# Performance work log

Measured on AMD Instinct MI355X. Metric: run time of the kernel, lower is better.

## Reference

```python
import jax, jax.numpy as jnp
import numpy as np

N = 50000       # nodes
E = 800000      # edges (before self-loops)
IN_DIM = 128
HID = 64
HEADS = 4
C = HID // HEADS  # 16 per-head channels
NEG_SLOPE = 0.2   # PyG GATConv default
BN_EPS = 1e-5


def setup_inputs() -> dict:
    key = jax.random.key(0)
    ks = jax.random.split(key, 16)
    inp = {
        "x": jax.random.normal(ks[0], (N, IN_DIM), jnp.float32),
        "edge_index": jax.random.randint(ks[1], (2, E), 0, N, dtype=jnp.int32),
    }
    def glorot(k, shape):
        fan = sum(shape)
        return jax.random.normal(k, shape, jnp.float32) * jnp.sqrt(2.0 / fan)
    # layer 0: in=IN_DIM, layer 1: in=HID
    inp["W0"] = glorot(ks[2], (IN_DIM, HEADS * C))
    inp["a_src0"] = glorot(ks[3], (HEADS, C))
    inp["a_dst0"] = glorot(ks[4], (HEADS, C))
    inp["b0"] = jnp.zeros((HEADS * C,), jnp.float32)
    inp["g0"] = jnp.ones((HID,), jnp.float32)
    inp["be0"] = jnp.zeros((HID,), jnp.float32)
    inp["W1"] = glorot(ks[5], (HID, HEADS * C))
    inp["a_src1"] = glorot(ks[6], (HEADS, C))
    inp["a_dst1"] = glorot(ks[7], (HEADS, C))
    inp["b1"] = jnp.zeros((HEADS * C,), jnp.float32)
    inp["g1"] = jnp.ones((HID,), jnp.float32)
    inp["be1"] = jnp.zeros((HID,), jnp.float32)
    return inp


def _segment_softmax(e, dst, n):
    # softmax over edges grouped by destination node, per head. e: [Et, H]
    m = jax.ops.segment_max(e, dst, num_segments=n)          # [N, H]
    ex = jnp.exp(e - m[dst])
    s = jax.ops.segment_sum(ex, dst, num_segments=n)         # [N, H]
    return ex / (s[dst] + 1e-16)


def _gat_conv(h, src, dst, W, a_s, a_d, b):
    n = h.shape[0]
    hp = (h @ W).reshape(n, HEADS, C)                        # [N, H, C]
    al_s = jnp.einsum('nhc,hc->nh', hp, a_s)                 # [N, H]
    al_d = jnp.einsum('nhc,hc->nh', hp, a_d)
    e = jax.nn.leaky_relu(al_s[src] + al_d[dst], NEG_SLOPE)  # [Et, H]
    alpha = _segment_softmax(e, dst, n)
    msg = hp[src] * alpha[:, :, None]                        # [Et, H, C]
    out = jax.ops.segment_sum(msg, dst, num_segments=n)      # [N, H, C]
    return out.reshape(n, HEADS * C) + b


def _batch_norm(h, g, b):
    mu = h.mean(axis=0)
    var = h.var(axis=0)
    return (h - mu) * jax.lax.rsqrt(var + BN_EPS) * g + b


def reference(x, edge_index, W0, a_src0, a_dst0, b0, g0, be0,
              W1, a_src1, a_dst1, b1, g1, be1):
    n = x.shape[0]
    loops = jnp.arange(n, dtype=edge_index.dtype)
    src = jnp.concatenate([edge_index[0], loops])  # PyG adds self-loops
    dst = jnp.concatenate([edge_index[1], loops])
    h = _gat_conv(x, src, dst, W0, a_src0, a_dst0, b0)
    h = _batch_norm(h, g0, be0)
    h = jax.nn.relu(h)  # dropout: identity (eval / deterministic)
    h = _gat_conv(h, src, dst, W1, a_src1, a_dst1, b1)
    h = _batch_norm(h, g1, be1)
    return h
```

## Files before the change

### kernel.cpp

```cpp
#include <hip/hip_runtime.h>

#define CAP 128

template<int K, bool APPLY_BN>
__global__ void __launch_bounds__(256, 4)
gemm_tiled(const float* __restrict__ X, const float* __restrict__ W,
           const float* __restrict__ a_s, const float* __restrict__ a_d,
           const float* __restrict__ scale, const float* __restrict__ shift,
           float* __restrict__ hp, float* __restrict__ al_s,
           float* __restrict__ al_d, int n)
{
  __shared__ float Wl[(K / 4) * 64 * 4];
  __shared__ float Xt[64 * K];

  for (int g = threadIdx.x; g < (K / 4) * 64; g += 256) {
    int k4 = g >> 6, ln = g & 63;
    float4 w;
    w.x = W[(k4 * 4 + 0) * 64 + ln];
    w.y = W[(k4 * 4 + 1) * 64 + ln];
    w.z = W[(k4 * 4 + 2) * 64 + ln];
    w.w = W[(k4 * 4 + 3) * 64 + ln];
    *(float4*)&Wl[g * 4] = w;
  }

  int row0 = blockIdx.x * 64;
  int nrows = min(64, n - row0);
  float4 sc, sh;
  if (APPLY_BN) {
    sc = *(const float4*)&scale[(threadIdx.x & 15) * 4];
    sh = *(const float4*)&shift[(threadIdx.x & 15) * 4];
  }
  const float4* src = (const float4*)(X + (size_t)row0 * K);
  int nf4 = nrows * (K / 4);
  for (int i = threadIdx.x; i < nf4; i += 256) {
    float4 v = src[i];
    if (APPLY_BN) {
      v.x = fmaxf(v.x * sc.x + sh.x, 0.f);
      v.y = fmaxf(v.y * sc.y + sh.y, 0.f);
      v.z = fmaxf(v.z * sc.z + sh.z, 0.f);
      v.w = fmaxf(v.w * sc.w + sh.w, 0.f);
    }
    *(float4*)&Xt[i * 4] = v;
  }
  __syncthreads();

  int lane = threadIdx.x & 63;
  int wid  = threadIdx.x >> 6;
  int rbase = wid * 16;
  float acc[16];
#pragma unroll
  for (int r = 0; r < 16; ++r) acc[r] = 0.f;

  for (int k4 = 0; k4 < K / 4; ++k4) {
    float4 wv = *(const float4*)&Wl[(k4 * 64 + lane) * 4];
#pragma unroll
    for (int r = 0; r < 16; ++r) {
      float4 xv = *(const float4*)&Xt[(rbase + r) * K + k4 * 4];
      acc[r] += xv.x * wv.x + xv.y * wv.y + xv.z * wv.z + xv.w * wv.w;
    }
  }

  float as_l = a_s[lane], ad_l = a_d[lane];
  int h = lane >> 4, c = lane & 15;
#pragma unroll
  for (int r = 0; r < 16; ++r) {
    int lr = rbase + r;
    if (lr >= nrows) break;
    int row = row0 + lr;
    float a = acc[r];
    hp[(size_t)row * 64 + lane] = a;
    float vs = a * as_l;
    float vd = a * ad_l;
#pragma unroll
    for (int off = 8; off >= 1; off >>= 1) {
      vs += __shfl_xor(vs, off, 64);
      vd += __shfl_xor(vd, off, 64);
    }
    if (c == 0) { al_s[row * 4 + h] = vs; al_d[row * 4 + h] = vd; }
  }
}

__global__ void bn_coeffs(const float* __restrict__ bnsum, const float* __restrict__ bnsq,
                          const float* __restrict__ g, const float* __restrict__ be,
                          float* __restrict__ scale, float* __restrict__ shift, int n)
{
  int c = threadIdx.x;
  float inv_n = 1.f / (float)n;
  float mu  = bnsum[c] * inv_n;
  float var = bnsq[c] * inv_n - mu * mu;
  float s = g[c] * rsqrtf(var + 1e-5f);
  scale[c] = s;
  shift[c] = be[c] - mu * s;
}

__global__ void hist_k(const int* __restrict__ ei, int E, int N, int* __restrict__ count)
{
  int e = blockIdx.x * 256 + threadIdx.x;
  int Et = E + N;
  if (e >= Et) return;
  int d = (e < E) ? ei[E + e] : (e - E);
  atomicAdd(&count[d], 1);
}

__global__ void scan_block_k(const int* __restrict__ count, int* __restrict__ row_ptr,
                             int* __restrict__ partial, int n)
{
  __shared__ int woff[16];
  int tid = threadIdx.x;
  int i = blockIdx.x * 1024 + tid;
  int v = (i < n) ? count[i] : 0;
  int lane = tid & 63, wid = tid >> 6;
  int incl = v;
#pragma unroll
  for (int off = 1; off < 64; off <<= 1) {
    int t = __shfl_up(incl, off, 64);
    if (lane >= off) incl += t;
  }
  if (lane == 63) woff[wid] = incl;
  __syncthreads();
  if (tid < 16) {
    int wv = woff[tid];
    int winc = wv;
#pragma unroll
    for (int off = 1; off < 16; off <<= 1) {
      int t = __shfl_up(winc, off, 64);
      if (tid >= off) winc += t;
    }
    woff[tid] = winc - wv;
    if (tid == 15) partial[blockIdx.x] = winc;
  }
  __syncthreads();
  if (i < n) row_ptr[i] = woff[wid] + incl - v;
}

__global__ void scan_partial_k(int* __restrict__ partial, int* __restrict__ row_ptr,
                               int nb, int n)
{
  int tid = threadIdx.x;
  int v = (tid < nb) ? partial[tid] : 0;
  int incl = v;
#pragma unroll
  for (int off = 1; off < 64; off <<= 1) {
    int t = __shfl_up(incl, off, 64);
    if (tid >= off) incl += t;
  }
  if (tid < nb) partial[tid] = incl - v;
  if (tid == 63) row_ptr[n] = incl;
}

__global__ void scan_add_k(int* __restrict__ row_ptr, int* __restrict__ cursor,
                           const int* __restrict__ partial, int n)
{
  int i = blockIdx.x * 1024 + threadIdx.x;
  if (i < n) {
    int r = row_ptr[i] + partial[blockIdx.x];
    row_ptr[i] = r;
    cursor[i] = r;
  }
}

__global__ void scatter_k(const int* __restrict__ ei, int E, int N,
                          int* __restrict__ cursor, int* __restrict__ col_src)
{
  int e = blockIdx.x * 256 + threadIdx.x;
  int Et = E + N;
  if (e >= Et) return;
  int s, d;
  if (e < E) { s = ei[e]; d = ei[E + e]; } else { s = d = e - E; }
  int pos = atomicAdd(&cursor[d], 1);
  col_src[pos] = s;
}

__global__ void __launch_bounds__(256)
node_agg(const int* __restrict__ row_ptr, const int* __restrict__ col_src,
         const float* __restrict__ hp, const float* __restrict__ al_s,
         const float* __restrict__ al_d, const float* __restrict__ bias,
         float* __restrict__ hpre, float* __restrict__ bnsum, float* __restrict__ bnsq,
         int n)
{
  __shared__ float sh_ex[4][CAP * 4];
  __shared__ int   sh_s[4][CAP];
  __shared__ float shs[64], shq[64];

  int lane = threadIdx.x & 63;
  int wid  = threadIdx.x >> 6;
  int h    = lane >> 4;
  float b  = bias[lane];
  float lsum = 0.f, lsq = 0.f;
  int nwaves = gridDim.x * 4;

  for (int d = blockIdx.x * 4 + wid; d < n; d += nwaves) {
    int beg = row_ptr[d], end = row_ptr[d + 1];
    int deg = end - beg;
    const float4 ald4 = *(const float4*)(al_d + (size_t)d * 4);
    float outv;

    if (deg <= CAP) {
      float mx = -1e30f, my = -1e30f, mz = -1e30f, mw = -1e30f;
      for (int jb = 0; jb < deg; jb += 64) {
        int jj = jb + lane;
        float ex = -1e30f, ey = -1e30f, ez = -1e30f, ew = -1e30f;
        if (jj < deg) {
          int s = col_src[beg + jj];
          float4 as4 = *(const float4*)(al_s + (size_t)s * 4);
          ex = as4.x + ald4.x; ex = ex >= 0.f ? ex : 0.2f * ex;
          ey = as4.y + ald4.y; ey = ey >= 0.f ? ey : 0.2f * ey;
          ez = as4.z + ald4.z; ez = ez >= 0.f ? ez : 0.2f * ez;
          ew = as4.w + ald4.w; ew = ew >= 0.f ? ew : 0.2f * ew;
          sh_s[wid][jj] = s;
          *(float4*)&sh_ex[wid][jj * 4] = make_float4(ex, ey, ez, ew);
        }
        mx = fmaxf(mx, ex); my = fmaxf(my, ey);
        mz = fmaxf(mz, ez); mw = fmaxf(mw, ew);
      }
#pragma unroll
      for (int off = 32; off >= 1; off >>= 1) {
        mx = fmaxf(mx, __shfl_xor(mx, off, 64));
        my = fmaxf(my, __shfl_xor(my, off, 64));
        mz = fmaxf(mz, __shfl_xor(mz, off, 64));
        mw = fmaxf(mw, __shfl_xor(mw, off, 64));
      }
      float sx = 0.f, sy = 0.f, sz = 0.f, sw = 0.f;
      for (int jb = 0; jb < deg; jb += 64) {
        int jj = jb + lane;
        if (jj < deg) {
          float4* p = (float4*)&sh_ex[wid][jj * 4];
          float4 eb = *p;
          eb.x = __expf(eb.x - mx); eb.y = __expf(eb.y - my);
          eb.z = __expf(eb.z - mz); eb.w = __expf(eb.w - mw);
          *p = eb;
          sx += eb.x; sy += eb.y; sz += eb.z; sw += eb.w;
        }
      }
#pragma unroll
      for (int off = 32; off >= 1; off >>= 1) {
        sx += __shfl_xor(sx, off, 64);
        sy += __shfl_xor(sy, off, 64);
        sz += __shfl_xor(sz, off, 64);
        sw += __shfl_xor(sw, off, 64);
      }
      float denom = (h == 0) ? sx : (h == 1) ? sy : (h == 2) ? sz : sw;
      float acc = 0.f;
      int jj = 0;
      for (; jj + 4 <= deg; jj += 4) {
        int s0 = sh_s[wid][jj],     s1 = sh_s[wid][jj + 1];
        int s2 = sh_s[wid][jj + 2], s3 = sh_s[wid][jj + 3];
        float e0 = sh_ex[wid][jj * 4 + h],       e1 = sh_ex[wid][(jj + 1) * 4 + h];
        float e2 = sh_ex[wid][(jj + 2) * 4 + h], e3 = sh_ex[wid][(jj + 3) * 4 + h];
        acc += e0 * hp[(size_t)s0 * 64 + lane];
        acc += e1 * hp[(size_t)s1 * 64 + lane];
        acc += e2 * hp[(size_t)s2 * 64 + lane];
        acc += e3 * hp[(size_t)s3 * 64 + lane];
      }
      for (; jj < deg; ++jj)
        acc += sh_ex[wid][jj * 4 + h] * hp[(size_t)sh_s[wid][jj] * 64 + lane];
      outv = acc / (denom + 1e-16f) + b;
    } else {
      float ald_h = (h == 0) ? ald4.x : (h == 1) ? ald4.y : (h == 2) ? ald4.z : ald4.w;
      float m = -1e30f;
      for (int j = beg; j < end; ++j) {
        int s = col_src[j];
        float v = al_s[s * 4 + h] + ald_h;
        v = (v >= 0.f) ? v : 0.2f * v;
        m = fmaxf(m, v);
      }
      float acc = 0.f, sum = 0.f;
      for (int j = beg; j < end; ++j) {
        int s = col_src[j];
        float v = al_s[s * 4 + h] + ald_h;
        v = (v >= 0.f) ? v : 0.2f * v;
        float ex2 = __expf(v - m);
        sum += ex2;
        acc += ex2 * hp[(size_t)s * 64 + lane];
      }
      outv = acc / (sum + 1e-16f) + b;
    }
    hpre[(size_t)d * 64 + lane] = outv;
    lsum += outv; lsq += outv * outv;
  }

  if (threadIdx.x < 64) { shs[threadIdx.x] = 0.f; shq[threadIdx.x] = 0.f; }
  __syncthreads();
  atomicAdd(&shs[lane], lsum);
  atomicAdd(&shq[lane], lsq);
  __syncthreads();
  if (threadIdx.x < 64) {
    atomicAdd(&bnsum[threadIdx.x], shs[threadIdx.x]);
    atomicAdd(&bnsq[threadIdx.x],  shq[threadIdx.x]);
  }
}

__global__ void bn_apply(const float* __restrict__ hpre, const float* __restrict__ bnsum,
                         const float* __restrict__ bnsq, const float* __restrict__ g,
                         const float* __restrict__ be, float* __restrict__ out, int n)
{
  size_t i = (size_t)blockIdx.x * 256 + threadIdx.x;
  size_t total = (size_t)n * 64;
  if (i >= total) return;
  int c = (int)(i & 63);
  float inv_n = 1.f / (float)n;
  float mu  = bnsum[c] * inv_n;
  float var = bnsq[c] * inv_n - mu * mu;
  out[i] = (hpre[i] - mu) * rsqrtf(var + 1e-5f) * g[c] + be[c];
}

extern "C" void kernel_launch(void* const* d_in, const int* in_sizes, int n_in,
                              void* d_out, int out_size, void* d_ws, size_t ws_size,
                              hipStream_t stream) {
  const float* x   = (const float*)d_in[0];
  const int*   ei  = (const int*)d_in[1];
  const float* W0  = (const float*)d_in[2];
  const float* as0 = (const float*)d_in[3];
  const float* ad0 = (const float*)d_in[4];
  const float* b0  = (const float*)d_in[5];
  const float* g0  = (const float*)d_in[6];
  const float* be0 = (const float*)d_in[7];
  const float* W1  = (const float*)d_in[8];
  const float* as1 = (const float*)d_in[9];
  const float* ad1 = (const float*)d_in[10];
  const float* b1  = (const float*)d_in[11];
  const float* g1  = (const float*)d_in[12];
  const float* be1 = (const float*)d_in[13];
  float* out = (float*)d_out;

  int N = in_sizes[0] / 128;
  int E = in_sizes[1] / 2;
  int Et = E + N;

  char* w = (char*)d_ws;
  auto alloc = [&](size_t bytes) {
    char* p = w; w += (bytes + 255) & ~255ull; return p;
  };
  float* hp    = (float*)alloc((size_t)N * 64 * 4);
  float* hpre0 = (float*)alloc((size_t)N * 64 * 4);
  float* hpre1 = (float*)alloc((size_t)N * 64 * 4);
  float* als   = (float*)alloc((size_t)N * 4 * 4);
  float* ald   = (float*)alloc((size_t)N * 4 * 4);
  int*   count = (int*)alloc((size_t)N * 4);
  int*   rowp  = (int*)alloc((size_t)(N + 1) * 4);
  int*   cursor= (int*)alloc((size_t)N * 4);
  int*   parts = (int*)alloc(64 * 4);
  int*   csrc  = (int*)alloc((size_t)Et * 4);
  float* bnsum = (float*)alloc(64 * 4);
  float* bnsq  = (float*)alloc(64 * 4);
  float* scale = (float*)alloc(64 * 4);
  float* shift = (float*)alloc(64 * 4);

  dim3 blk(256);
  int gEt   = (Et + 255) / 256;
  int gN64  = (N * 64 + 255) / 256;
  int nb    = (N + 1023) / 1024;
  int gTile = (N + 63) / 64;

  hipMemsetAsync(count, 0, (size_t)N * 4, stream);
  hist_k<<<gEt, blk, 0, stream>>>(ei, E, N, count);
  scan_block_k<<<nb, 1024, 0, stream>>>(count, rowp, parts, N);
  scan_partial_k<<<1, 64, 0, stream>>>(parts, rowp, nb, N);
  scan_add_k<<<nb, 1024, 0, stream>>>(rowp, cursor, parts, N);
  scatter_k<<<gEt, blk, 0, stream>>>(ei, E, N, cursor, csrc);

  hipMemsetAsync(bnsum, 0, 64 * 4, stream);
  hipMemsetAsync(bnsq,  0, 64 * 4, stream);
  gemm_tiled<128, false><<<gTile, blk, 0, stream>>>(x, W0, as0, ad0, nullptr, nullptr,
                                                    hp, als, ald, N);
  node_agg<<<2048, blk, 0, stream>>>(rowp, csrc, hp, als, ald, b0,
                                     hpre0, bnsum, bnsq, N);
  bn_coeffs<<<1, 64, 0, stream>>>(bnsum, bnsq, g0, be0, scale, shift, N);

  hipMemsetAsync(bnsum, 0, 64 * 4, stream);
  hipMemsetAsync(bnsq,  0, 64 * 4, stream);
  gemm_tiled<64, true><<<gTile, blk, 0, stream>>>(hpre0, W1, as1, ad1, scale, shift,
                                                  hp, als, ald, N);
  node_agg<<<2048, blk, 0, stream>>>(rowp, csrc, hp, als, ald, b1,
                                     hpre1, bnsum, bnsq, N);
  bn_apply<<<gN64, blk, 0, stream>>>(hpre1, bnsum, bnsq, g1, be1, out, N);
}
```

Measured before the change: 349.8 us.

## Store hp in fp16, drop softmax max pass, fuse BN coeffs into GEMM

Stores the projected features hp as half precision to halve the bytes gathered in aggregation. It removes the segment-max pass and exponentiates the raw logits directly, merging the logit and exp loops. It folds the bn_coeffs kernel into the second GEMM prologue and unrolls the gather loop by 8. The changes risk fp16 rounding error and exp overflow for large logits, since the max subtraction is gone.

New measurement: 329.7 us. 5.8% less time.

```diff
diff --git a/kernel.cpp b/kernel.cpp
--- a/kernel.cpp
+++ b/kernel.cpp
@@ -1,4 +1,5 @@
 #include <hip/hip_runtime.h>
+#include <hip/hip_fp16.h>
 
 #define CAP 128
 
@@ -6,29 +7,38 @@
 __global__ void __launch_bounds__(256, 4)
 gemm_tiled(const float* __restrict__ X, const float* __restrict__ W,
            const float* __restrict__ a_s, const float* __restrict__ a_d,
-           const float* __restrict__ scale, const float* __restrict__ shift,
-           float* __restrict__ hp, float* __restrict__ al_s,
+           const float* __restrict__ bnsum, const float* __restrict__ bnsq,
+           const float* __restrict__ g, const float* __restrict__ be,
+           __half* __restrict__ hp, float* __restrict__ al_s,
            float* __restrict__ al_d, int n)
 {
   __shared__ float Wl[(K / 4) * 64 * 4];
   __shared__ float Xt[64 * K];
 
-  for (int g = threadIdx.x; g < (K / 4) * 64; g += 256) {
-    int k4 = g >> 6, ln = g & 63;
+  for (int gi = threadIdx.x; gi < (K / 4) * 64; gi += 256) {
+    int k4 = gi >> 6, ln = gi & 63;
     float4 w;
     w.x = W[(k4 * 4 + 0) * 64 + ln];
     w.y = W[(k4 * 4 + 1) * 64 + ln];
     w.z = W[(k4 * 4 + 2) * 64 + ln];
     w.w = W[(k4 * 4 + 3) * 64 + ln];
-    *(float4*)&Wl[g * 4] = w;
+    *(float4*)&Wl[gi * 4] = w;
   }
 
   int row0 = blockIdx.x * 64;
   int nrows = min(64, n - row0);
   float4 sc, sh;
   if (APPLY_BN) {
-    sc = *(const float4*)&scale[(threadIdx.x & 15) * 4];
-    sh = *(const float4*)&shift[(threadIdx.x & 15) * 4];
+    int cg = (threadIdx.x & 15) * 4;
+    float inv_n = 1.f / (float)n;
+#pragma unroll
+    for (int q = 0; q < 4; ++q) {
+      float mu  = bnsum[cg + q] * inv_n;
+      float var = bnsq[cg + q] * inv_n - mu * mu;
+      float s   = g[cg + q] * rsqrtf(var + 1e-5f);
+      ((float*)&sc)[q] = s;
+      ((float*)&sh)[q] = be[cg + q] - mu * s;
+    }
   }
   const float4* src = (const float4*)(X + (size_t)row0 * K);
   int nf4 = nrows * (K / 4);
@@ -68,7 +78,7 @@
     if (lr >= nrows) break;
     int row = row0 + lr;
     float a = acc[r];
-    hp[(size_t)row * 64 + lane] = a;
+    hp[(size_t)row * 64 + lane] = __float2half(a);
     float vs = a * as_l;
     float vd = a * ad_l;
 #pragma unroll
@@ -78,19 +88,6 @@
     }
     if (c == 0) { al_s[row * 4 + h] = vs; al_d[row * 4 + h] = vd; }
   }
-}
-
-__global__ void bn_coeffs(const float* __restrict__ bnsum, const float* __restrict__ bnsq,
-                          const float* __restrict__ g, const float* __restrict__ be,
-                          float* __restrict__ scale, float* __restrict__ shift, int n)
-{
-  int c = threadIdx.x;
-  float inv_n = 1.f / (float)n;
-  float mu  = bnsum[c] * inv_n;
-  float var = bnsq[c] * inv_n - mu * mu;
-  float s = g[c] * rsqrtf(var + 1e-5f);
-  scale[c] = s;
-  shift[c] = be[c] - mu * s;
 }
 
 __global__ void hist_k(const int* __restrict__ ei, int E, int N, int* __restrict__ count)
@@ -173,7 +170,7 @@
 
 __global__ void __launch_bounds__(256)
 node_agg(const int* __restrict__ row_ptr, const int* __restrict__ col_src,
-         const float* __restrict__ hp, const float* __restrict__ al_s,
+         const __half* __restrict__ hp, const float* __restrict__ al_s,
          const float* __restrict__ al_d, const float* __restrict__ bias,
          float* __restrict__ hpre, float* __restrict__ bnsum, float* __restrict__ bnsq,
          int n)
@@ -196,40 +193,20 @@
     float outv;
 
     if (deg <= CAP) {
-      float mx = -1e30f, my = -1e30f, mz = -1e30f, mw = -1e30f;
-      for (int jb = 0; jb < deg; jb += 64) {
-        int jj = jb + lane;
-        float ex = -1e30f, ey = -1e30f, ez = -1e30f, ew = -1e30f;
-        if (jj < deg) {
-          int s = col_src[beg + jj];
-          float4 as4 = *(const float4*)(al_s + (size_t)s * 4);
-          ex = as4.x + ald4.x; ex = ex >= 0.f ? ex : 0.2f * ex;
-          ey = as4.y + ald4.y; ey = ey >= 0.f ? ey : 0.2f * ey;
-          ez = as4.z + ald4.z; ez = ez >= 0.f ? ez : 0.2f * ez;
-          ew = as4.w + ald4.w; ew = ew >= 0.f ? ew : 0.2f * ew;
-          sh_s[wid][jj] = s;
-          *(float4*)&sh_ex[wid][jj * 4] = make_float4(ex, ey, ez, ew);
-        }
-        mx = fmaxf(mx, ex); my = fmaxf(my, ey);
-        mz = fmaxf(mz, ez); mw = fmaxf(mw, ew);
-      }
-#pragma unroll
-      for (int off = 32; off >= 1; off >>= 1) {
-        mx = fmaxf(mx, __shfl_xor(mx, off, 64));
-        my = fmaxf(my, __shfl_xor(my, off, 64));
-        mz = fmaxf(mz, __shfl_xor(mz, off, 64));
-        mw = fmaxf(mw, __shfl_xor(mw, off, 64));
-      }
       float sx = 0.f, sy = 0.f, sz = 0.f, sw = 0.f;
       for (int jb = 0; jb < deg; jb += 64) {
         int jj = jb + lane;
         if (jj < deg) {
-          float4* p = (float4*)&sh_ex[wid][jj * 4];
-          float4 eb = *p;
-          eb.x = __expf(eb.x - mx); eb.y = __expf(eb.y - my);
-          eb.z = __expf(eb.z - mz); eb.w = __expf(eb.w - mw);
-          *p = eb;
-          sx += eb.x; sy += eb.y; sz += eb.z; sw += eb.w;
+          int s = col_src[beg + jj];
+          float4 as4 = *(const float4*)(al_s + (size_t)s * 4);
+          float ex = as4.x + ald4.x; ex = ex >= 0.f ? ex : 0.2f * ex;
+          float ey = as4.y + ald4.y; ey = ey >= 0.f ? ey : 0.2f * ey;
+          float ez = as4.z + ald4.z; ez = ez >= 0.f ? ez : 0.2f * ez;
+          float ew = as4.w + ald4.w; ew = ew >= 0.f ? ew : 0.2f * ew;
+          ex = __expf(ex); ey = __expf(ey); ez = __expf(ez); ew = __expf(ew);
+          sh_s[wid][jj] = s;
+          *(float4*)&sh_ex[wid][jj * 4] = make_float4(ex, ey, ez, ew);
+          sx += ex; sy += ey; sz += ez; sw += ew;
         }
       }
 #pragma unroll
@@ -242,36 +219,52 @@
       float denom = (h == 0) ? sx : (h == 1) ? sy : (h == 2) ? sz : sw;
       float acc = 0.f;
       int jj = 0;
+      for (; jj + 8 <= deg; jj += 8) {
+        int s0 = sh_s[wid][jj],     s1 = sh_s[wid][jj + 1];
+        int s2 = sh_s[wid][jj + 2], s3 = sh_s[wid][jj + 3];
+        int s4 = sh_s[wid][jj + 4], s5 = sh_s[wid][jj + 5];
+        int s6 = sh_s[wid][jj + 6], s7 = sh_s[wid][jj + 7];
+        float e0 = sh_ex[wid][(jj + 0) * 4 + h], e1 = sh_ex[wid][(jj + 1) * 4 + h];
+        float e2 = sh_ex[wid][(jj + 2) * 4 + h], e3 = sh_ex[wid][(jj + 3) * 4 + h];
+        float e4 = sh_ex[wid][(jj + 4) * 4 + h], e5 = sh_ex[wid][(jj + 5) * 4 + h];
+        float e6 = sh_ex[wid][(jj + 6) * 4 + h], e7 = sh_ex[wid][(jj + 7) * 4 + h];
+        acc += e0 * __half2float(hp[(size_t)s0 * 64 + lane]);
+        acc += e1 * __half2float(hp[(size_t)s1 * 64 + lane]);
+        acc += e2 * __half2float(hp[(size_t)s2 * 64 + lane]);
+        acc += e3 * __half2float(hp[(size_t)s3 * 64 + lane]);
+        acc += e4 * __half2float(hp[(size_t)s4 * 64 + lane]);
+        acc += e5 * __half2float(hp[(size_t)s5 * 64 + lane]);
+        acc += e6 * __half2float(hp[(size_t)s6 * 64 + lane]);
+        acc += e7 * __half2float(hp[(size_t)s7 * 64 + lane]);
+      }
       for (; jj + 4 <= deg; jj += 4) {
         int s0 = sh_s[wid][jj],     s1 = sh_s[wid][jj + 1];
         int s2 = sh_s[wid][jj + 2], s3 = sh_s[wid][jj + 3];
-        float e0 = sh_ex[wid][jj * 4 + h],       e1 = sh_ex[wid][(jj + 1) * 4 + h];
+        float e0 = sh_ex[wid][(jj + 0) * 4 + h], e1 = sh_ex[wid][(jj + 1) * 4 + h];
         float e2 = sh_ex[wid][(jj + 2) * 4 + h], e3 = sh_ex[wid][(jj + 3) * 4 + h];
-        acc += e0 * hp[(size_t)s0 * 64 + lane];
-        acc += e1 * hp[(size_t)s1 * 64 + lane];
-        acc += e2 * hp[(size_t)s2 * 64 + lane];
-        acc += e3 * hp[(size_t)s3 * 64 + lane];
+        acc += e0 * __half2float(hp[(size_t)s0 * 64 + lane]);
+        acc += e1 * __half2float(hp[(size_t)s1 * 64 + lane]);
+        acc += e2 * __half2float(hp[(size_t)s2 * 64 + lane]);
+        acc += e3 * __half2float(hp[(size_t)s3 * 64 + lane]);
       }
       for (; jj < deg; ++jj)
-        acc += sh_ex[wid][jj * 4 + h] * hp[(size_t)sh_s[wid][jj] * 64 + lane];
+        acc += sh_ex[wid][jj * 4 + h] * __half2float(hp[(size_t)sh_s[wid][jj] * 64 + lane]);
       outv = acc / (denom + 1e-16f) + b;
     } else {
       float ald_h = (h == 0) ? ald4.x : (h == 1) ? ald4.y : (h == 2) ? ald4.z : ald4.w;
-      float m = -1e30f;
+      float sum = 0.f;
       for (int j = beg; j < end; ++j) {
         int s = col_src[j];
         float v = al_s[s * 4 + h] + ald_h;
         v = (v >= 0.f) ? v : 0.2f * v;
-        m = fmaxf(m, v);
-      }
-      float acc = 0.f, sum = 0.f;
+        sum += __expf(v);
+      }
+      float acc = 0.f;
       for (int j = beg; j < end; ++j) {
         int s = col_src[j];
         float v = al_s[s * 4 + h] + ald_h;
         v = (v >= 0.f) ? v : 0.2f * v;
-        float ex2 = __expf(v - m);
-        sum += ex2;
-        acc += ex2 * hp[(size_t)s * 64 + lane];
+        acc += __expf(v) * __half2float(hp[(size_t)s * 64 + lane]);
       }
       outv = acc / (sum + 1e-16f) + b;
     }
@@ -331,20 +324,18 @@
   auto alloc = [&](size_t bytes) {
     char* p = w; w += (bytes + 255) & ~255ull; return p;
   };
-  float* hp    = (float*)alloc((size_t)N * 64 * 4);
-  float* hpre0 = (float*)alloc((size_t)N * 64 * 4);
-  float* hpre1 = (float*)alloc((size_t)N * 64 * 4);
-  float* als   = (float*)alloc((size_t)N * 4 * 4);
-  float* ald   = (float*)alloc((size_t)N * 4 * 4);
-  int*   count = (int*)alloc((size_t)N * 4);
-  int*   rowp  = (int*)alloc((size_t)(N + 1) * 4);
-  int*   cursor= (int*)alloc((size_t)N * 4);
-  int*   parts = (int*)alloc(64 * 4);
-  int*   csrc  = (int*)alloc((size_t)Et * 4);
-  float* bnsum = (float*)alloc(64 * 4);
-  float* bnsq  = (float*)alloc(64 * 4);
-  float* scale = (float*)alloc(64 * 4);
-  float* shift = (float*)alloc(64 * 4);
+  __half* hp    = (__half*)alloc((size_t)N * 64 * 2);
+  float*  hpre0 = (float*)alloc((size_t)N * 64 * 4);
+  float*  hpre1 = (float*)alloc((size_t)N * 64 * 4);
+  float*  als   = (float*)alloc((size_t)N * 4 * 4);
+  float*  ald   = (float*)alloc((size_t)N * 4 * 4);
+  int*    count = (int*)alloc((size_t)N * 4);
+  int*    rowp  = (int*)alloc((size_t)(N + 1) * 4);
+  int*    cursor= (int*)alloc((size_t)N * 4);
+  int*    parts = (int*)alloc(64 * 4);
+  int*    csrc  = (int*)alloc((size_t)Et * 4);
+  float*  bnsum = (float*)alloc(64 * 4);
+  float*  bnsq  = (float*)alloc(64 * 4);
 
   dim3 blk(256);
   int gEt   = (Et + 255) / 256;
@@ -361,16 +352,17 @@
 
   hipMemsetAsync(bnsum, 0, 64 * 4, stream);
   hipMemsetAsync(bnsq,  0, 64 * 4, stream);
-  gemm_tiled<128, false><<<gTile, blk, 0, stream>>>(x, W0, as0, ad0, nullptr, nullptr,
+  gemm_tiled<128, false><<<gTile, blk, 0, stream>>>(x, W0, as0, ad0,
+                                                    nullptr, nullptr, nullptr, nullptr,
                                                     hp, als, ald, N);
   node_agg<<<2048, blk, 0, stream>>>(rowp, csrc, hp, als, ald, b0,
                                      hpre0, bnsum, bnsq, N);
-  bn_coeffs<<<1, 64, 0, stream>>>(bnsum, bnsq, g0, be0, scale, shift, N);
-
+
+  gemm_tiled<64, true><<<gTile, blk, 0, stream>>>(hpre0, W1, as1, ad1,
+                                                  bnsum, bnsq, g0, be0,
+                                                  hp, als, ald, N);
   hipMemsetAsync(bnsum, 0, 64 * 4, stream);
   hipMemsetAsync(bnsq,  0, 64 * 4, stream);
-  gemm_tiled<64, true><<<gTile, blk, 0, stream>>>(hpre0, W1, as1, ad1, scale, shift,
-                                                  hp, als, ald, N);
   node_agg<<<2048, blk, 0, stream>>>(rowp, csrc, hp, als, ald, b1,
                                      hpre1, bnsum, bnsq, N);
   bn_apply<<<gN64, blk, 0, stream>>>(hpre1, bnsum, bnsq, g1, be1, out, N);
```
